# Kernel tuning notes

Hardware: AMD Instinct MI355X
Metric: run time of the kernel (lower is better)

Reference implementation:

```python
import jax, jax.numpy as jnp
import numpy as np

N = 4096          # num_nodes
B = 16            # num_graphs (equal-sized contiguous segments)
L = 2             # max degree -> (L+1)**2 = 9 spherical components
NUM_DEG = (L + 1) ** 2
F = 128           # input feature dim
FQK = 128         # query/key feature dim
FV = 128          # value feature dim
MAX_FREQ = 8.0
MAX_LEN = 10.0

# degree index of each spherical component: [0, 1,1,1, 2,2,2,2,2]
DEG_IDX = np.array([l for l in range(L + 1) for _ in range(2 * l + 1)], dtype=np.int32)
# Lebedev grid num=6: octahedron vertices, equal weights 1/6
GRID_U = np.array([[1, 0, 0], [-1, 0, 0], [0, 1, 0], [0, -1, 0], [0, 0, 1], [0, 0, -1]], dtype=np.float32)
GRID_W = np.full((6,), 1.0 / 6.0, dtype=np.float32)


def _edense(x, W, b, deg_idx):
    y = jnp.einsum('npmf,mfg->npmg', x, W[deg_idx])
    return y.at[:, :, 0, :].add(b)


def _erope(x, cos, sin):
    # x: (N, 1, M9, Fqk); cos/sin: (N, G, H) with H = Fqk // 2
    x1 = x[:, None, :, :, 0::2]  # (N,1,1,M9,H) -> broadcast over G
    x2 = x[:, None, :, :, 1::2]
    c = cos[:, :, None, None, :]
    s = sin[:, :, None, None, :]
    r1 = x1 * c - x2 * s
    r2 = x1 * s + x2 * c
    out = jnp.stack([r1, r2], axis=-1)  # interleave pairs back
    return out.reshape(out.shape[:-2] + (-1,))  # (N, G, 1, M9, Fqk)


def setup_inputs() -> dict:
    key = jax.random.key(0)
    ks = jax.random.split(key, 8)
    inputs = jax.random.normal(ks[0], (N, 1, NUM_DEG, F), jnp.float32)
    positions = jax.random.normal(ks[1], (N, 3), jnp.float32) * 3.0
    # contiguous equal-sized graph segments (jraph-style padding convention)
    batch_segments = jnp.repeat(jnp.arange(B), N // B)
    graph_mask = jnp.ones((B,), bool)
    s = 1.0 / np.sqrt(F)
    Wq = jax.random.normal(ks[2], (L + 1, F, FQK), jnp.float32) * s
    Wk = jax.random.normal(ks[3], (L + 1, F, FQK), jnp.float32) * s
    Wv = jax.random.normal(ks[4], (L + 1, F, FV), jnp.float32) * s
    bq = jnp.zeros((FQK,), jnp.float32)
    bk = jnp.zeros((FQK,), jnp.float32)
    bv = jnp.zeros((FV,), jnp.float32)
    return dict(inputs=inputs, positions=positions, batch_segments=batch_segments,
                graph_mask=graph_mask, Wq=Wq, bq=bq, Wk=Wk, bk=bk, Wv=Wv, bv=bv)


def reference(inputs, positions, batch_segments, graph_mask, Wq, bq, Wk, bk, Wv, bv):
    deg_idx = jnp.asarray(DEG_IDX)
    grid_u = jnp.asarray(GRID_U)
    grid_w = jnp.asarray(GRID_W)
    G = grid_u.shape[0]
    # frequencies per frequency_init_fn: linspace(0, max_freq, Fqk/2) / max_length
    theta = jnp.linspace(0.0, MAX_FREQ, FQK // 2, dtype=jnp.float32) / MAX_LEN  # (H,)

    q = _edense(inputs, Wq, bq, deg_idx)  # (N,1,M9,FQK)
    k = _edense(inputs, Wk, bk, deg_idx)
    v = _edense(inputs, Wv, bv, deg_idx)  # (N,1,M9,FV)

    # Euclidean RoPE phases: angle[n,g,h] = (pos_n . u_g) * theta_h
    phase = positions @ grid_u.T           # (N,G)
    ang = phase[:, :, None] * theta        # (N,G,H)
    cos, sin = jnp.cos(ang), jnp.sin(ang)

    Mdim = NUM_DEG * FQK
    Ddim = NUM_DEG * FV
    qr = _erope(q, cos, sin).reshape(N, G, Mdim)  # (N,G,M)
    kr = _erope(k, cos, sin).reshape(N, G, Mdim)
    vf = v.reshape(N, Ddim)

    # per-graph linear attention with Lebedev quadrature (contiguous equal segments)
    n = N // B
    qr_b = qr.reshape(B, n, G, Mdim)
    kr_b = kr.reshape(B, n, G, Mdim)
    v_b = vf.reshape(B, n, Ddim)
    kv = jnp.einsum('bngm,bnd->bgmd', kr_b, v_b)          # KV summaries
    kv = kv * grid_w[None, :, None, None]                 # quadrature weights
    out = jnp.einsum('bngm,bgmd->bnd', qr_b, kv)          # integrate over grid
    out = out.reshape(N, 1, NUM_DEG, FV)
    mask = graph_mask[batch_segments]                     # (N,)
    return jnp.where(mask[:, None, None, None], out, 0.0)
```

## Files before the change

### kernel.cpp

```cpp
#include <hip/hip_runtime.h>


typedef unsigned short u16;
typedef __attribute__((ext_vector_type(8))) short short8;
typedef __attribute__((ext_vector_type(4))) float f32x4;
typedef __attribute__((ext_vector_type(4))) unsigned short u16x4;

static constexpr int N_NODES = 4096;
static constexpr int NBATCH  = 16;
static constexpr int NB      = 256;
static constexpr int NDEG    = 9;
static constexpr int MD      = NDEG * 128;
static constexpr int KTOT    = 6 * MD;
static constexpr size_t ASLICE = (size_t)NBATCH * NB * NB;

static constexpr size_t OFF_WT  = 0;
static constexpr size_t OFF_QR  = OFF_WT  + (size_t)9*16384*2;
static constexpr size_t OFF_KR  = OFF_QR  + (size_t)N_NODES*KTOT*2;
static constexpr size_t OFF_VT  = OFF_KR  + (size_t)N_NODES*KTOT*2;
static constexpr size_t OFF_AP  = OFF_VT  + (size_t)N_NODES*MD*2;

__device__ inline u16 f2bf(float x) {
    union { float f; unsigned u; } v; v.f = x;
    unsigned r = v.u + 0x7fffu + ((v.u >> 16) & 1u);
    return (u16)(r >> 16);
}
__device__ inline float bf2f(u16 h) {
    union { unsigned u; float f; } v; v.u = ((unsigned)h) << 16; return v.f;
}

__global__ __launch_bounds__(256) void k_prep(const float* __restrict__ Wq,
                                              const float* __restrict__ Wk,
                                              const float* __restrict__ Wv,
                                              u16* __restrict__ wt) {
    int t = blockIdx.x, tid = threadIdx.x;
    int blk = t >> 2, tt = t & 3;
    int mat = blk / 3, l = blk % 3;
    const float* W = (mat == 0 ? Wq : (mat == 1 ? Wk : Wv)) + (size_t)l * 16384;
    int j0 = (tt >> 1) * 64, f0 = (tt & 1) * 64;
    __shared__ u16 tile[64 * 72];
    for (int e = tid; e < 1024; e += 256) {
        int r = e >> 4, c = e & 15;
        float4 wv = *(const float4*)(W + (size_t)(f0 + r) * 128 + j0 + c * 4);
        tile[(c * 4 + 0) * 72 + r] = f2bf(wv.x);
        tile[(c * 4 + 1) * 72 + r] = f2bf(wv.y);
        tile[(c * 4 + 2) * 72 + r] = f2bf(wv.z);
        tile[(c * 4 + 3) * 72 + r] = f2bf(wv.w);
    }
    __syncthreads();
    u16* dst = wt + (size_t)blk * 16384;
    for (int e = tid; e < 512; e += 256) {
        int j = e >> 3, c = e & 7;
        *(uint4*)(dst + (size_t)(j0 + j) * 128 + f0 + c * 8) = *(const uint4*)(tile + j * 72 + c * 8);
    }
}

__global__ __launch_bounds__(256) void k_qkv(const float* __restrict__ X,
                                             const u16* __restrict__ wt,
                                             const float* __restrict__ bq,
                                             const float* __restrict__ bk,
                                             const float* __restrict__ bv,
                                             const float* __restrict__ pos,
                                             u16* __restrict__ qr,
                                             u16* __restrict__ kr,
                                             u16* __restrict__ vt) {
    const int nt = blockIdx.x, m = blockIdx.y, mat = blockIdx.z;
    const int n0 = nt * 64;
    const int deg = (m == 0) ? 0 : (m < 4 ? 1 : 2);
    const int tid = threadIdx.x;

    __shared__ u16 smem[26112];
    __shared__ float posS[192];
    u16* Xs = smem;
    u16* Ws = smem + 64 * 136;

    if (tid < 192) posS[tid] = pos[(size_t)n0 * 3 + tid];

    for (int e = tid; e < 2048; e += 256) {
        int r = e >> 5, f4 = e & 31;
        float4 xv = *(const float4*)(X + (size_t)(n0 + r) * MD + m * 128 + f4 * 4);
        u16x4 o; o.x = f2bf(xv.x); o.y = f2bf(xv.y); o.z = f2bf(xv.z); o.w = f2bf(xv.w);
        *(u16x4*)(Xs + r * 136 + f4 * 4) = o;
    }
    {
        const uint4* wsrc = (const uint4*)(wt + (size_t)(mat * 3 + deg) * 16384);
        for (int e = tid; e < 2048; e += 256) {
            int j = e >> 4, f8 = e & 15;
            *(uint4*)(Ws + j * 136 + f8 * 8) = wsrc[j * 16 + f8];
        }
    }
    __syncthreads();

    const int w = tid >> 6, lane = tid & 63, quad = lane >> 4, lrow = lane & 15;
    f32x4 acc[8];
#pragma unroll
    for (int ct = 0; ct < 8; ct++) acc[ct] = (f32x4){0.f, 0.f, 0.f, 0.f};
#pragma unroll
    for (int ks = 0; ks < 4; ks++) {
        short8 a = *(const short8*)(Xs + (w * 16 + lrow) * 136 + ks * 32 + quad * 8);
#pragma unroll
        for (int ct = 0; ct < 8; ct++) {
            short8 bfr = *(const short8*)(Ws + (ct * 16 + lrow) * 136 + ks * 32 + quad * 8);
            acc[ct] = __builtin_amdgcn_mfma_f32_16x16x32_bf16(a, bfr, acc[ct], 0, 0, 0);
        }
    }

    const float* bias = (mat == 0) ? bq : ((mat == 1) ? bk : bv);
    float yv[8][4];
#pragma unroll
    for (int ct = 0; ct < 8; ct++) {
        float bj = (m == 0) ? bias[ct * 16 + lrow] : 0.0f;
#pragma unroll
        for (int r = 0; r < 4; r++) yv[ct][r] = acc[ct][r] + bj;
    }

    if (mat == 2) {
        u16* T = Ws;
        __syncthreads();
#pragma unroll
        for (int ct = 0; ct < 8; ct++)
#pragma unroll
            for (int r = 0; r < 4; r++) {
                int nl = w * 16 + quad * 4 + r;
                T[(ct * 16 + lrow) * 66 + nl] = f2bf(yv[ct][r]);
            }
        __syncthreads();
        for (int e = tid; e < 1024; e += 256) {
            int d = e >> 3, c = e & 7;
            *(uint4*)(vt + (size_t)(m * 128 + d) * N_NODES + n0 + c * 8) =
                *(const uint4*)(T + d * 66 + c * 8);
        }
        return;
    }

    float pv[8][4];
#pragma unroll
    for (int ct = 0; ct < 8; ct++)
#pragma unroll
        for (int r = 0; r < 4; r++) pv[ct][r] = __shfl_xor(yv[ct][r], 1);

    float pr[4][3];
#pragma unroll
    for (int r = 0; r < 4; r++) {
        int nl = w * 16 + quad * 4 + r;
#pragma unroll
        for (int gp = 0; gp < 3; gp++) pr[r][gp] = posS[nl * 3 + gp];
    }
    const float thq = (float)(lrow >> 1) * (8.0f / 630.0f);
    const float th8 = 8.0f * (8.0f / 630.0f);

    u16* O0 = Xs;
    u16* O1 = Ws;
    u16* dst = (mat == 0) ? qr : kr;
    const bool even = !(lrow & 1);

    for (int gp = 0; gp < 3; gp++) {
        __syncthreads();
#pragma unroll
        for (int ct = 0; ct < 8; ct++) {
            float th = thq + (float)ct * th8;
#pragma unroll
            for (int r = 0; r < 4; r++) {
                int nl = w * 16 + quad * 4 + r;
                float s, c;
                __sincosf(pr[r][gp] * th, &s, &c);
                float t1 = yv[ct][r] * c, t2 = pv[ct][r] * s;
                float r0, r1;
                if (even) { r0 = t1 - t2; r1 = t1 + t2; }
                else      { r0 = t1 + t2; r1 = t1 - t2; }
                O0[nl * 136 + ct * 16 + lrow] = f2bf(r0);
                O1[nl * 136 + ct * 16 + lrow] = f2bf(r1);
            }
        }
        __syncthreads();
        for (int e = tid; e < 1024; e += 256) {
            int nl = e >> 4, c = e & 15;
            size_t o0 = ((size_t)(gp * 2) * N_NODES + n0 + nl) * MD + m * 128 + c * 8;
            *(uint4*)(dst + o0)                      = *(const uint4*)(O0 + nl * 136 + c * 8);
            *(uint4*)(dst + o0 + (size_t)N_NODES*MD) = *(const uint4*)(O1 + nl * 136 + c * 8);
        }
    }
}

__global__ __launch_bounds__(256) void k_gemm1(const u16* __restrict__ qr,
                                               const u16* __restrict__ kr,
                                               u16* __restrict__ Apart) {
    int t = blockIdx.x, b = blockIdx.y, g = blockIdx.z;
    int tr = t >> 2, tc = t & 3;
    int qn0 = b * NB + tr * 64, kn0 = b * NB + tc * 64;
    const size_t gbase = (size_t)g * N_NODES;
    int tid = threadIdx.x;
    __shared__ u16 Qs[64 * 72];
    __shared__ u16 Ks[64 * 72];
    int w = tid >> 6, lane = tid & 63, quad = lane >> 4, lrow = lane & 15;

    f32x4 acc[4];
#pragma unroll
    for (int ct = 0; ct < 4; ct++) acc[ct] = (f32x4){0.f, 0.f, 0.f, 0.f};

    for (int kc = 0; kc < MD / 64; kc++) {
        int k0 = kc * 64;
#pragma unroll
        for (int e = tid; e < 512; e += 256) {
            int r = e >> 3, s = e & 7;
            *(uint4*)(Qs + r * 72 + s * 8) = *(const uint4*)(qr + (gbase + qn0 + r) * MD + k0 + s * 8);
            *(uint4*)(Ks + r * 72 + s * 8) = *(const uint4*)(kr + (gbase + kn0 + r) * MD + k0 + s * 8);
        }
        __syncthreads();
#pragma unroll
        for (int ks = 0; ks < 2; ks++) {
            short8 a = *(const short8*)(Qs + (w * 16 + lrow) * 72 + ks * 32 + quad * 8);
#pragma unroll
            for (int ct = 0; ct < 4; ct++) {
                short8 bfr = *(const short8*)(Ks + (ct * 16 + lrow) * 72 + ks * 32 + quad * 8);
                acc[ct] = __builtin_amdgcn_mfma_f32_16x16x32_bf16(a, bfr, acc[ct], 0, 0, 0);
            }
        }
        __syncthreads();
    }
    u16* dst = Apart + ((size_t)g * NBATCH + b) * (NB * NB);
#pragma unroll
    for (int ct = 0; ct < 4; ct++)
#pragma unroll
        for (int r = 0; r < 4; r++) {
            int rib = tr * 64 + w * 16 + quad * 4 + r;
            int cib = tc * 64 + ct * 16 + lrow;
            dst[(size_t)rib * NB + cib] = f2bf(acc[ct][r]);
        }
}

__global__ __launch_bounds__(256) void k_gemm2(const u16* __restrict__ Ap,
                                               const u16* __restrict__ vt,
                                               const int* __restrict__ gmask,
                                               float* __restrict__ out) {
    int rt = blockIdx.x, dcb = blockIdx.y, b = blockIdx.z;
    int d0 = dcb * 128;
    int tid = threadIdx.x;
    __shared__ u16 As[64 * 72];
    __shared__ u16 Vs[128 * 72];
    int w = tid >> 6, lane = tid & 63, quad = lane >> 4, lrow = lane & 15;

    f32x4 acc[8];
#pragma unroll
    for (int ct = 0; ct < 8; ct++) acc[ct] = (f32x4){0.f, 0.f, 0.f, 0.f};

    const float sc6 = 1.0f / 6.0f;
    for (int kc = 0; kc < 4; kc++) {
        int k0 = kc * 64;
#pragma unroll
        for (int e = tid; e < 512; e += 256) {
            int r = e >> 3, c8 = e & 7;
            size_t off = (size_t)b * (NB * NB) + (size_t)(rt * 64 + r) * NB + k0 + c8 * 8;
            float sacc[8];
#pragma unroll
            for (int i = 0; i < 8; i++) sacc[i] = 0.f;
#pragma unroll
            for (int s = 0; s < 6; s++) {
                uint4 v = *(const uint4*)(Ap + (size_t)s * ASLICE + off);
                const unsigned* u = (const unsigned*)&v;
#pragma unroll
                for (int h = 0; h < 4; h++) {
                    sacc[h * 2]     += bf2f((u16)(u[h] & 0xffff));
                    sacc[h * 2 + 1] += bf2f((u16)(u[h] >> 16));
                }
            }
            u16 o[8];
#pragma unroll
            for (int i = 0; i < 8; i++) o[i] = f2bf(sacc[i] * sc6);
            *(uint4*)(As + r * 72 + c8 * 8) = *(const uint4*)o;
        }
#pragma unroll
        for (int e = tid; e < 1024; e += 256) {
            int rr = e >> 3, sc2 = e & 7;
            *(uint4*)(Vs + rr * 72 + sc2 * 8) =
                *(const uint4*)(vt + (size_t)(d0 + rr) * N_NODES + b * NB + k0 + sc2 * 8);
        }
        __syncthreads();
#pragma unroll
        for (int ks = 0; ks < 2; ks++) {
            short8 a = *(const short8*)(As + (w * 16 + lrow) * 72 + ks * 32 + quad * 8);
#pragma unroll
            for (int ct = 0; ct < 8; ct++) {
                short8 bfr = *(const short8*)(Vs + (ct * 16 + lrow) * 72 + ks * 32 + quad * 8);
                acc[ct] = __builtin_amdgcn_mfma_f32_16x16x32_bf16(a, bfr, acc[ct], 0, 0, 0);
            }
        }
        __syncthreads();
    }
    int mv = gmask[b];
#pragma unroll
    for (int ct = 0; ct < 8; ct++)
#pragma unroll
        for (int r = 0; r < 4; r++) {
            int node = b * NB + rt * 64 + w * 16 + quad * 4 + r;
            int d = d0 + ct * 16 + lrow;
            out[(size_t)node * MD + d] = mv ? acc[ct][r] : 0.0f;
        }
}

extern "C" void kernel_launch(void* const* d_in, const int* in_sizes, int n_in,
                              void* d_out, int out_size, void* d_ws, size_t ws_size,
                              hipStream_t stream) {
    (void)in_sizes; (void)n_in; (void)out_size; (void)ws_size;

    const float* X    = (const float*)d_in[0];
    const float* pos  = (const float*)d_in[1];
    const int*   gmask= (const int*)  d_in[3];
    const float* Wq   = (const float*)d_in[4];
    const float* bq   = (const float*)d_in[5];
    const float* Wk   = (const float*)d_in[6];
    const float* bk   = (const float*)d_in[7];
    const float* Wv   = (const float*)d_in[8];
    const float* bv   = (const float*)d_in[9];
    float* out = (float*)d_out;

    char* ws = (char*)d_ws;
    u16*   wt   = (u16*)  (ws + OFF_WT);
    u16*   qrp  = (u16*)  (ws + OFF_QR);
    u16*   krp  = (u16*)  (ws + OFF_KR);
    u16*   vtp  = (u16*)  (ws + OFF_VT);
    u16*   App  = (u16*)  (ws + OFF_AP);

    k_prep <<<dim3(36),         dim3(256), 0, stream>>>(Wq, Wk, Wv, wt);
    k_qkv  <<<dim3(64, 9, 3),   dim3(256), 0, stream>>>(X, wt, bq, bk, bv, pos, qrp, krp, vtp);
    k_gemm1<<<dim3(16, 16, 6),  dim3(256), 0, stream>>>(qrp, krp, App);
    k_gemm2<<<dim3(4, 9, 16),   dim3(256), 0, stream>>>(App, vtp, gmask, out);
}
```

Before: 186.3 us.

## Fuse weight conversion into QKV kernel and remap gemm1 block order for L2 locality

Removes the separate weight-prep kernel: each QKV block now reads the fp32 weights directly, converts them to bf16 and transposes them into shared memory itself. This saves one launch and a round trip through the workspace, but every block repeats the conversion and performs strided 2-byte LDS stores that may cause bank conflicts. Separately, gemm1 uses a 1D grid whose block index is swizzled so that concurrently running blocks share Q/K row tiles, aiming for better L2 reuse.

After: 187.2 us. About the same (+0.5%).

```diff
diff --git a/kernel.cpp b/kernel.cpp
--- a/kernel.cpp
+++ b/kernel.cpp
@@ -14,8 +14,7 @@
 static constexpr int KTOT    = 6 * MD;
 static constexpr size_t ASLICE = (size_t)NBATCH * NB * NB;
 
-static constexpr size_t OFF_WT  = 0;
-static constexpr size_t OFF_QR  = OFF_WT  + (size_t)9*16384*2;
+static constexpr size_t OFF_QR  = 0;
 static constexpr size_t OFF_KR  = OFF_QR  + (size_t)N_NODES*KTOT*2;
 static constexpr size_t OFF_VT  = OFF_KR  + (size_t)N_NODES*KTOT*2;
 static constexpr size_t OFF_AP  = OFF_VT  + (size_t)N_NODES*MD*2;
@@ -29,34 +28,10 @@
     union { unsigned u; float f; } v; v.u = ((unsigned)h) << 16; return v.f;
 }
 
-__global__ __launch_bounds__(256) void k_prep(const float* __restrict__ Wq,
-                                              const float* __restrict__ Wk,
-                                              const float* __restrict__ Wv,
-                                              u16* __restrict__ wt) {
-    int t = blockIdx.x, tid = threadIdx.x;
-    int blk = t >> 2, tt = t & 3;
-    int mat = blk / 3, l = blk % 3;
-    const float* W = (mat == 0 ? Wq : (mat == 1 ? Wk : Wv)) + (size_t)l * 16384;
-    int j0 = (tt >> 1) * 64, f0 = (tt & 1) * 64;
-    __shared__ u16 tile[64 * 72];
-    for (int e = tid; e < 1024; e += 256) {
-        int r = e >> 4, c = e & 15;
-        float4 wv = *(const float4*)(W + (size_t)(f0 + r) * 128 + j0 + c * 4);
-        tile[(c * 4 + 0) * 72 + r] = f2bf(wv.x);
-        tile[(c * 4 + 1) * 72 + r] = f2bf(wv.y);
-        tile[(c * 4 + 2) * 72 + r] = f2bf(wv.z);
-        tile[(c * 4 + 3) * 72 + r] = f2bf(wv.w);
-    }
-    __syncthreads();
-    u16* dst = wt + (size_t)blk * 16384;
-    for (int e = tid; e < 512; e += 256) {
-        int j = e >> 3, c = e & 7;
-        *(uint4*)(dst + (size_t)(j0 + j) * 128 + f0 + c * 8) = *(const uint4*)(tile + j * 72 + c * 8);
-    }
-}
-
 __global__ __launch_bounds__(256) void k_qkv(const float* __restrict__ X,
-                                             const u16* __restrict__ wt,
+                                             const float* __restrict__ Wq,
+                                             const float* __restrict__ Wk,
+                                             const float* __restrict__ Wv,
                                              const float* __restrict__ bq,
                                              const float* __restrict__ bk,
                                              const float* __restrict__ bv,
@@ -83,10 +58,14 @@
         *(u16x4*)(Xs + r * 136 + f4 * 4) = o;
     }
     {
-        const uint4* wsrc = (const uint4*)(wt + (size_t)(mat * 3 + deg) * 16384);
-        for (int e = tid; e < 2048; e += 256) {
-            int j = e >> 4, f8 = e & 15;
-            *(uint4*)(Ws + j * 136 + f8 * 8) = wsrc[j * 16 + f8];
+        const float* Wsrc = (mat == 0 ? Wq : (mat == 1 ? Wk : Wv)) + (size_t)deg * 16384;
+        for (int e = tid; e < 4096; e += 256) {
+            int f = e >> 5, jc = e & 31;
+            float4 wv = *(const float4*)(Wsrc + (size_t)f * 128 + jc * 4);
+            Ws[(jc * 4 + 0) * 136 + f] = f2bf(wv.x);
+            Ws[(jc * 4 + 1) * 136 + f] = f2bf(wv.y);
+            Ws[(jc * 4 + 2) * 136 + f] = f2bf(wv.z);
+            Ws[(jc * 4 + 3) * 136 + f] = f2bf(wv.w);
         }
     }
     __syncthreads();
@@ -185,8 +164,16 @@
 __global__ __launch_bounds__(256) void k_gemm1(const u16* __restrict__ qr,
                                                const u16* __restrict__ kr,
                                                u16* __restrict__ Apart) {
-    int t = blockIdx.x, b = blockIdx.y, g = blockIdx.z;
-    int tr = t >> 2, tc = t & 3;
+    int idx = blockIdx.x;
+    int grp = idx >> 6;
+    int sub = idx & 63;
+    int c   = sub & 7;
+    int j   = sub >> 3;
+    int bg  = grp * 4 + (c & 3);
+    int g   = bg >> 4, b = bg & 15;
+    int tr  = (c >> 2) * 2 + (j & 1);
+    int tc  = j >> 1;
+
     int qn0 = b * NB + tr * 64, kn0 = b * NB + tc * 64;
     const size_t gbase = (size_t)g * N_NODES;
     int tid = threadIdx.x;
@@ -315,14 +302,13 @@
     float* out = (float*)d_out;
 
     char* ws = (char*)d_ws;
-    u16*   wt   = (u16*)  (ws + OFF_WT);
     u16*   qrp  = (u16*)  (ws + OFF_QR);
     u16*   krp  = (u16*)  (ws + OFF_KR);
     u16*   vtp  = (u16*)  (ws + OFF_VT);
     u16*   App  = (u16*)  (ws + OFF_AP);
 
-    k_prep <<<dim3(36),         dim3(256), 0, stream>>>(Wq, Wk, Wv, wt);
-    k_qkv  <<<dim3(64, 9, 3),   dim3(256), 0, stream>>>(X, wt, bq, bk, bv, pos, qrp, krp, vtp);
-    k_gemm1<<<dim3(16, 16, 6),  dim3(256), 0, stream>>>(qrp, krp, App);
-    k_gemm2<<<dim3(4, 9, 16),   dim3(256), 0, stream>>>(App, vtp, gmask, out);
-}
+    k_qkv  <<<dim3(64, 9, 3),  dim3(256), 0, stream>>>(X, Wq, Wk, Wv, bq, bk, bv, pos,
+                                                       qrp, krp, vtp);
+    k_gemm1<<<dim3(1536),      dim3(256), 0, stream>>>(qrp, krp, App);
+    k_gemm2<<<dim3(4, 9, 16),  dim3(256), 0, stream>>>(App, vtp, gmask, out);
+}
```
